# Performance work log

Hardware: AMD Instinct MI355X
Metric: run time of the kernel (lower is better)

Reference implementation:

```python
import jax, jax.numpy as jnp
import numpy as np

N_NODES = 50000
N_EDGES = 800000
N_GRAPHS = 64
IN_CH = 128
HID_CH = 128
OUT_CH = 2


def setup_inputs() -> dict:
    key = jax.random.key(0)
    k = jax.random.split(key, 7)
    x = jax.random.normal(k[0], (N_NODES, IN_CH), dtype=jnp.float32)
    edge_index = jax.random.randint(k[1], (2, N_EDGES), 0, N_NODES, dtype=jnp.int64)
    batch = jnp.sort(jax.random.randint(k[2], (N_NODES,), 0, N_GRAPHS, dtype=jnp.int64))
    W1 = jax.random.normal(k[3], (IN_CH, HID_CH), dtype=jnp.float32) * 0.05
    b1 = jnp.zeros((HID_CH,), dtype=jnp.float32)
    W2 = jax.random.normal(k[4], (HID_CH, OUT_CH), dtype=jnp.float32) * 0.05
    b2 = jnp.zeros((OUT_CH,), dtype=jnp.float32)
    return {"x": x, "edge_index": edge_index, "batch": batch,
            "W1": W1, "b1": b1, "W2": W2, "b2": b2}


def gcn_conv(x, edge_index, W, b):
    """PyG GCNConv: add self-loops, symmetric D^{-1/2}(A+I)D^{-1/2} aggregation of XW, plus bias."""
    n = x.shape[0]
    loop = jnp.arange(n, dtype=edge_index.dtype)
    src = jnp.concatenate([edge_index[0], loop])  # [E+N]
    dst = jnp.concatenate([edge_index[1], loop])
    ones = jnp.ones_like(dst, dtype=x.dtype)
    deg = jax.ops.segment_sum(ones, dst, num_segments=n)      # in-degree incl. self-loop (>=1)
    d_inv_sqrt = jax.lax.rsqrt(deg)
    norm = d_inv_sqrt[src] * d_inv_sqrt[dst]                  # [E+N]
    h = x @ W                                                 # [N, out]
    msg = h[src] * norm[:, None]                              # gather + scale
    out = jax.ops.segment_sum(msg, dst, num_segments=n)       # scatter-add
    return out + b


def global_mean_pool(x, batch, num_graphs):
    sums = jax.ops.segment_sum(x, batch, num_segments=num_graphs)
    cnt = jax.ops.segment_sum(jnp.ones((x.shape[0],), dtype=x.dtype), batch, num_segments=num_graphs)
    return sums / jnp.maximum(cnt, 1.0)[:, None]


def reference(x, edge_index, batch, W1, b1, W2, b2):
    h = jax.nn.relu(gcn_conv(x, edge_index, W1, b1))
    h = gcn_conv(h, edge_index, W2, b2)
    out = global_mean_pool(h, batch, N_GRAPHS)  # [G, out_channels]
    # dropout in eval mode == identity
    return out
```

## Files before the change

### kernel.cpp

```cpp
#include <hip/hip_runtime.h>


#define NGRAPH 64
#define CH 128
#define BSUB 384
#define NCOPY 8
#define BCAPT (BSUB * NCOPY)
#define CSTR 4096

typedef float f32x4 __attribute__((ext_vector_type(4)));
typedef _Float16 f16x8 __attribute__((ext_vector_type(8)));
typedef _Float16 f16x4 __attribute__((ext_vector_type(4)));
typedef _Float16 f16x2 __attribute__((ext_vector_type(2)));

__global__ void k_init(int* __restrict__ bcur8, float* __restrict__ gsum,
                       int* __restrict__ gcnt, int* __restrict__ done,
                       float* __restrict__ h2,
                       const float* __restrict__ W1, _Float16* __restrict__ w1t,
                       int NB, int N) {
    int i = blockIdx.x * blockDim.x + threadIdx.x;
    if (i < NB * NCOPY) bcur8[i] = 0;
    if (i < 2 * NGRAPH) gsum[i] = 0.f;
    if (i < NGRAPH) gcnt[i] = 0;
    if (i == 0) *done = 0;
    if (i < 2) h2[2 * N + i] = 0.f;
    if (i < CH * CH) {
        int k = i >> 7, c = i & 127;
        w1t[c * CH + k] = (_Float16)W1[i];
    }
}

__global__ __launch_bounds__(256) void k_bin(const int* __restrict__ src,
                                             const int* __restrict__ dst,
                                             int* __restrict__ bcur8,
                                             unsigned int* __restrict__ tmp,
                                             int E, int EPB) {
    __shared__ int hist[512];
    __shared__ int gbase[512];
    __shared__ int cur[512];
    int t = threadIdx.x;
    int e0 = blockIdx.x * EPB;
    int e1 = min(E, e0 + EPB);
    for (int i = t; i < 512; i += 256) { hist[i] = 0; cur[i] = 0; }
    __syncthreads();
    for (int e = e0 + t; e < e1; e += 256)
        atomicAdd(&hist[dst[e] >> 7], 1);
    __syncthreads();
    int copy = blockIdx.x & (NCOPY - 1);
    for (int b = t; b < 512; b += 256) {
        int hc = hist[b];
        if (hc) gbase[b] = atomicAdd(&bcur8[b * NCOPY + copy], hc);
    }
    __syncthreads();
    for (int e = e0 + t; e < e1; e += 256) {
        int d = dst[e];
        int b = d >> 7;
        int li = atomicAdd(&cur[b], 1);
        int pos = gbase[b] + li;
        if (pos < BSUB)
            tmp[(size_t)b * BCAPT + copy * BSUB + pos] =
                ((unsigned)(d & 127) << 25) | (unsigned)src[e];
    }
}

__global__ __launch_bounds__(256) void k_build(const unsigned int* __restrict__ tmp,
                                               const int* __restrict__ bcur8,
                                               int2* __restrict__ rs2,
                                               float* __restrict__ dinv,
                                               int* __restrict__ csr, int N) {
    __shared__ int hist[128];
    __shared__ int scan[128];
    __shared__ int lcur[128];
    int b = blockIdx.x, t = threadIdx.x;
    if (t < 128) hist[t] = 0;
    __syncthreads();
    const unsigned int* tb = tmp + (size_t)b * BCAPT;
    for (int c = 0; c < NCOPY; c++) {
        int cnt = min(bcur8[b * NCOPY + c], BSUB);
        const unsigned int* tp = tb + c * BSUB;
        for (int e = t; e < cnt; e += 256) atomicAdd(&hist[tp[e] >> 25], 1);
    }
    __syncthreads();
    int val = 0, v = 0, pv = 0;
    if (t < 128) { v = hist[t]; pv = (v + 7) & ~7; val = pv; scan[t] = val; }
    __syncthreads();
    for (int off = 1; off < 128; off <<= 1) {
        int add = (t >= off && t < 128) ? scan[t - off] : 0;
        __syncthreads();
        if (t < 128) { val += add; scan[t] = val; }
        __syncthreads();
    }
    int base = b * CSTR;
    if (t < 128) {
        int excl = val - pv;
        lcur[t] = excl;
        int n = b * 128 + t;
        if (n < N) {
            rs2[n] = make_int2(base + excl, pv);
            dinv[n] = rsqrtf((float)(v + 1));
            for (int e = v; e < pv; e++) csr[base + excl + e] = N;
        }
    }
    __syncthreads();
    for (int c = 0; c < NCOPY; c++) {
        int cnt = min(bcur8[b * NCOPY + c], BSUB);
        const unsigned int* tp = tb + c * BSUB;
        for (int e = t; e < cnt; e += 256) {
            unsigned p = tp[e];
            int pos = atomicAdd(&lcur[p >> 25], 1);
            csr[base + pos] = (int)(p & 0x01FFFFFFu);
        }
    }
}

__global__ __launch_bounds__(256) void k_gemm1(const float* __restrict__ X,
                                               const _Float16* __restrict__ w1t,
                                               const float* __restrict__ dinv,
                                               _Float16* __restrict__ H, int N) {
    __shared__ _Float16 Xs[64 * 136];
    __shared__ _Float16 Ws[128 * 136];
    int t = threadIdx.x;
    int row0 = blockIdx.x * 64;
    const float4* Xv = (const float4*)X;

    #pragma unroll
    for (int i = 0; i < 8; i++) {
        int gi = t + i * 256;
        int r = gi >> 5, c4 = gi & 31;
        int gr = row0 + r;
        float4 v = (gr < N) ? Xv[(size_t)gr * 32 + c4] : make_float4(0.f, 0.f, 0.f, 0.f);
        f16x4 hv = {(_Float16)v.x, (_Float16)v.y, (_Float16)v.z, (_Float16)v.w};
        *(f16x4*)&Xs[r * 136 + 4 * c4] = hv;
    }
    #pragma unroll
    for (int i = 0; i < 8; i++) {
        int gi = t + i * 256;
        int r = gi >> 4, cc = gi & 15;
        f16x8 vv = *(const f16x8*)&w1t[r * CH + cc * 8];
        *(f16x8*)&Ws[r * 136 + cc * 8] = vv;
    }
    __syncthreads();

    int w = t >> 6, l = t & 63;
    int r0w = w * 16;
    int lr = l & 15, lk = (l >> 4) * 8;
    f32x4 acc[8] = {};
    #pragma unroll
    for (int k0 = 0; k0 < 128; k0 += 32) {
        f16x8 a = *(const f16x8*)&Xs[(r0w + lr) * 136 + k0 + lk];
        #pragma unroll
        for (int c = 0; c < 8; c++) {
            f16x8 bf = *(const f16x8*)&Ws[(c * 16 + lr) * 136 + k0 + lk];
            acc[c] = __builtin_amdgcn_mfma_f32_16x16x32_f16(a, bf, acc[c], 0, 0, 0);
        }
    }
    float dv[4];
    #pragma unroll
    for (int q = 0; q < 4; q++) {
        int gr = row0 + r0w + (l >> 4) * 4 + q;
        dv[q] = (gr < N) ? dinv[gr] : 0.f;
    }
    __syncthreads();
    #pragma unroll
    for (int c = 0; c < 8; c++)
        #pragma unroll
        for (int q = 0; q < 4; q++)
            Xs[(r0w + (l >> 4) * 4 + q) * 136 + c * 16 + lr] = (_Float16)(acc[c][q] * dv[q]);
    __syncthreads();
    f16x2* Hv = (f16x2*)H;
    #pragma unroll
    for (int i = 0; i < 16; i++) {
        int gi = t + i * 256;
        int r = gi >> 6, cp = gi & 63;
        int gr = row0 + r;
        Hv[(size_t)gr * 64 + cp] = *(f16x2*)&Xs[r * 136 + 2 * cp];
    }
}

__global__ __launch_bounds__(256) void k_layer1(const _Float16* __restrict__ h,
                                                const int* __restrict__ csr,
                                                const int2* __restrict__ rs2,
                                                const float* __restrict__ dinv,
                                                const float* __restrict__ b1,
                                                const float* __restrict__ W2,
                                                float* __restrict__ h2, int N) {
    int n = (blockIdx.x * 256 + threadIdx.x) >> 6;
    int l = threadIdx.x & 63;
    if (n >= N) return;
    const f16x2* hv = (const f16x2*)h;
    float dn = dinv[n];
    f16x2 self = hv[(size_t)n * 64 + l];
    float acc0 = (float)self.x, acc1 = (float)self.y;
    int2 rs = rs2[n];
    int base = rs.x, cnt = rs.y;
    for (int c0 = 0; c0 < cnt; c0 += 64) {
        int m = cnt - c0; if (m > 64) m = 64;
        int idx = csr[base + c0 + l];
        for (int j = 0; j < m; j += 8) {
            int s0 = __shfl(idx, j + 0), s1 = __shfl(idx, j + 1);
            int s2 = __shfl(idx, j + 2), s3 = __shfl(idx, j + 3);
            int s4 = __shfl(idx, j + 4), s5 = __shfl(idx, j + 5);
            int s6 = __shfl(idx, j + 6), s7 = __shfl(idx, j + 7);
            f16x2 v0 = hv[(size_t)s0 * 64 + l];
            f16x2 v1 = hv[(size_t)s1 * 64 + l];
            f16x2 v2 = hv[(size_t)s2 * 64 + l];
            f16x2 v3 = hv[(size_t)s3 * 64 + l];
            f16x2 v4 = hv[(size_t)s4 * 64 + l];
            f16x2 v5 = hv[(size_t)s5 * 64 + l];
            f16x2 v6 = hv[(size_t)s6 * 64 + l];
            f16x2 v7 = hv[(size_t)s7 * 64 + l];
            acc0 += (float)v0.x; acc1 += (float)v0.y;
            acc0 += (float)v1.x; acc1 += (float)v1.y;
            acc0 += (float)v2.x; acc1 += (float)v2.y;
            acc0 += (float)v3.x; acc1 += (float)v3.y;
            acc0 += (float)v4.x; acc1 += (float)v4.y;
            acc0 += (float)v5.x; acc1 += (float)v5.y;
            acc0 += (float)v6.x; acc1 += (float)v6.y;
            acc0 += (float)v7.x; acc1 += (float)v7.y;
        }
    }
    float2 bb = ((const float2*)b1)[l];
    float v0 = fmaxf(fmaf(dn, acc0, bb.x), 0.f);
    float v1 = fmaxf(fmaf(dn, acc1, bb.y), 0.f);
    float4 w2 = ((const float4*)W2)[l];
    float p0 = fmaf(v0, w2.x, v1 * w2.z);
    float p1 = fmaf(v0, w2.y, v1 * w2.w);
    #pragma unroll
    for (int off = 32; off; off >>= 1) {
        p0 += __shfl_xor(p0, off);
        p1 += __shfl_xor(p1, off);
    }
    if (l == 0) ((float2*)h2)[n] = make_float2(p0 * dn, p1 * dn);
}

__global__ __launch_bounds__(256) void k_layer2_pool(const float* __restrict__ h2,
                                                     const int* __restrict__ csr,
                                                     const int2* __restrict__ rs2,
                                                     const float* __restrict__ dinv,
                                                     const int* __restrict__ batch,
                                                     float* __restrict__ gsum,
                                                     int* __restrict__ gcnt,
                                                     int* __restrict__ done,
                                                     const float* __restrict__ b2,
                                                     float* __restrict__ out, int N) {
    __shared__ float ssum[2 * NGRAPH];
    __shared__ int scnt[NGRAPH];
    __shared__ int s_last;
    int t = threadIdx.x;
    if (t < 2 * NGRAPH) ssum[t] = 0.f;
    if (t < NGRAPH) scnt[t] = 0;
    __syncthreads();
    int n = blockIdx.x * blockDim.x + t;
    if (n < N) {
        const float2* h2v = (const float2*)h2;
        float dn = dinv[n];
        float2 a = h2v[n];
        int2 rs = rs2[n];
        for (int e = rs.x; e < rs.x + rs.y; e++) {
            float2 v = h2v[csr[e]];
            a.x += v.x;
            a.y += v.y;
        }
        a.x *= dn;
        a.y *= dn;
        int g = batch[n];
        atomicAdd(&ssum[g * 2 + 0], a.x);
        atomicAdd(&ssum[g * 2 + 1], a.y);
        atomicAdd(&scnt[g], 1);
    }
    __syncthreads();
    if (t < 2 * NGRAPH) atomicAdd(&gsum[t], ssum[t]);
    if (t < NGRAPH) atomicAdd(&gcnt[t], scnt[t]);
    __syncthreads();
    if (t == 0) {
        __threadfence();
        int r = atomicAdd(done, 1);
        s_last = (r == (int)gridDim.x - 1) ? 1 : 0;
    }
    __syncthreads();
    if (s_last && t < 2 * NGRAPH) {
        int g = t >> 1, c = t & 1;
        float sv = atomicAdd(&gsum[t], 0.f);
        float cv = (float)atomicAdd(&gcnt[g], 0);
        out[t] = sv / fmaxf(cv, 1.f) + b2[c];
    }
}

extern "C" void kernel_launch(void* const* d_in, const int* in_sizes, int n_in,
                              void* d_out, int out_size, void* d_ws, size_t ws_size,
                              hipStream_t stream) {
    const float* x     = (const float*)d_in[0];
    const int*   ei    = (const int*)d_in[1];
    const int*   batch = (const int*)d_in[2];
    const float* W1    = (const float*)d_in[3];
    const float* b1    = (const float*)d_in[4];
    const float* W2    = (const float*)d_in[5];
    const float* b2    = (const float*)d_in[6];
    float* out = (float*)d_out;

    int N = in_sizes[0] / CH;
    int E = in_sizes[1] / 2;
    int NB = (N + 127) / 128;
    const int* esrc = ei;
    const int* edst = ei + E;

    char* w = (char*)d_ws;
    auto alloc = [&](size_t bytes) -> void* {
        void* p = (void*)w;
        w += (bytes + 255) & ~(size_t)255;
        return p;
    };
    _Float16* h      = (_Float16*)alloc((size_t)(N + 64) * CH * sizeof(_Float16));
    float* dinv      = (float*)alloc((size_t)N * sizeof(float));
    int2* rs2        = (int2*) alloc((size_t)N * sizeof(int2));
    int* csr         = (int*)  alloc((size_t)NB * CSTR * sizeof(int));
    float* h2        = (float*)alloc((size_t)(N + 1) * 2 * sizeof(float));
    int* bcur8       = (int*)  alloc((size_t)NB * NCOPY * sizeof(int));
    _Float16* w1t    = (_Float16*)alloc((size_t)CH * CH * sizeof(_Float16));
    float* gsum      = (float*)alloc(128 * sizeof(float));
    int* gcnt        = (int*)  alloc(64 * sizeof(int));
    int* done        = (int*)  alloc(256);
    unsigned int* tmp = (unsigned int*)h;

    int nbN = (N + 255) / 256;
    int NCHUNK = 256;
    int EPB = (E + NCHUNK - 1) / NCHUNK;

    k_init  <<<64, 256, 0, stream>>>(bcur8, gsum, gcnt, done, h2, W1, w1t, NB, N);
    k_bin   <<<NCHUNK, 256, 0, stream>>>(esrc, edst, bcur8, tmp, E, EPB);
    k_build <<<NB, 256, 0, stream>>>(tmp, bcur8, rs2, dinv, csr, N);
    k_gemm1 <<<(N + 63) / 64, 256, 0, stream>>>(x, w1t, dinv, h, N);
    k_layer1<<<(N * 64 + 255) / 256, 256, 0, stream>>>(h, csr, rs2, dinv, b1, W2, h2, N);
    k_layer2_pool<<<nbN, 256, 0, stream>>>(h2, csr, rs2, dinv, batch, gsum, gcnt,
                                           done, b2, out, N);
}
```

Measured before the change: 169.7 us.

## Fuse all GCN stages into one cooperative persistent kernel with grid barriers

The six separate launches (init, bin, build, gemm1, layer1, layer2+pool) become a single cooperative kernel of 512 blocks. Stages are separated by a hand-written atomic grid barrier, and control buffers are zeroed by one memset. The aim is to remove per-launch overhead and idle gaps between the small stages. Alongside this, the binning gets 16 copies of smaller sub-buckets, the edge scratch buffer is no longer aliased onto h, and gemm1 reads W1 fragments straight from global memory instead of staging them in LDS. In exchange there are barrier spin costs, a fixed grid that splits the gemm tiles unevenly, and a fallback multi-kernel path if the cooperative launch fails.

After: 474.5 us. 180% more time.

```diff
diff --git a/kernel.cpp b/kernel.cpp
--- a/kernel.cpp
+++ b/kernel.cpp
@@ -3,82 +3,77 @@
 
 #define NGRAPH 64
 #define CH 128
-#define BSUB 384
-#define NCOPY 8
+#define NTHR 256
+#define NBLK 512
+#define NCOPY 16
+#define BSUB 224
 #define BCAPT (BSUB * NCOPY)
-#define CSTR 4096
+#define CSTR 4608
 
 typedef float f32x4 __attribute__((ext_vector_type(4)));
 typedef _Float16 f16x8 __attribute__((ext_vector_type(8)));
 typedef _Float16 f16x4 __attribute__((ext_vector_type(4)));
 typedef _Float16 f16x2 __attribute__((ext_vector_type(2)));
 
-__global__ void k_init(int* __restrict__ bcur8, float* __restrict__ gsum,
-                       int* __restrict__ gcnt, int* __restrict__ done,
-                       float* __restrict__ h2,
-                       const float* __restrict__ W1, _Float16* __restrict__ w1t,
-                       int NB, int N) {
-    int i = blockIdx.x * blockDim.x + threadIdx.x;
-    if (i < NB * NCOPY) bcur8[i] = 0;
-    if (i < 2 * NGRAPH) gsum[i] = 0.f;
-    if (i < NGRAPH) gcnt[i] = 0;
-    if (i == 0) *done = 0;
-    if (i < 2) h2[2 * N + i] = 0.f;
-    if (i < CH * CH) {
-        int k = i >> 7, c = i & 127;
-        w1t[c * CH + k] = (_Float16)W1[i];
-    }
-}
-
-__global__ __launch_bounds__(256) void k_bin(const int* __restrict__ src,
-                                             const int* __restrict__ dst,
-                                             int* __restrict__ bcur8,
-                                             unsigned int* __restrict__ tmp,
-                                             int E, int EPB) {
-    __shared__ int hist[512];
-    __shared__ int gbase[512];
-    __shared__ int cur[512];
+struct MegaP {
+    const float* x; const int* esrc; const int* edst; const int* batch;
+    const float* W1; const float* b1; const float* W2; const float* b2;
+    float* out;
+    _Float16* h; unsigned int* tmp; float* dinv; int2* rs2; int* csr;
+    float* h2; int* bcur8; _Float16* w1t; float* gsum; int* gcnt; int* cnt;
+    int N, E, NB, EPB;
+};
+
+__device__ __forceinline__ void gbar(int* cnt, int ph) {
+    __syncthreads();
+    if (threadIdx.x == 0) {
+        __builtin_amdgcn_fence(__ATOMIC_RELEASE, "");
+        __hip_atomic_fetch_add(cnt, 1, __ATOMIC_RELAXED, __HIP_MEMORY_SCOPE_AGENT);
+        while (__hip_atomic_load(cnt, __ATOMIC_RELAXED, __HIP_MEMORY_SCOPE_AGENT)
+               < NBLK * ph)
+            __builtin_amdgcn_s_sleep(16);
+        __builtin_amdgcn_fence(__ATOMIC_ACQUIRE, "");
+    }
+    __syncthreads();
+}
+
+__device__ __forceinline__ void bin_body(const int* src, const int* dst,
+                                         int* bcur8, unsigned int* tmp,
+                                         int E, int e0, int e1, int copy,
+                                         int* hist, int* gbase, int* cur) {
     int t = threadIdx.x;
-    int e0 = blockIdx.x * EPB;
-    int e1 = min(E, e0 + EPB);
-    for (int i = t; i < 512; i += 256) { hist[i] = 0; cur[i] = 0; }
-    __syncthreads();
-    for (int e = e0 + t; e < e1; e += 256)
+    for (int i = t; i < 512; i += NTHR) { hist[i] = 0; cur[i] = 0; }
+    __syncthreads();
+    for (int e = e0 + t; e < e1; e += NTHR)
         atomicAdd(&hist[dst[e] >> 7], 1);
     __syncthreads();
-    int copy = blockIdx.x & (NCOPY - 1);
-    for (int b = t; b < 512; b += 256) {
+    for (int b = t; b < 512; b += NTHR) {
         int hc = hist[b];
         if (hc) gbase[b] = atomicAdd(&bcur8[b * NCOPY + copy], hc);
     }
     __syncthreads();
-    for (int e = e0 + t; e < e1; e += 256) {
+    for (int e = e0 + t; e < e1; e += NTHR) {
         int d = dst[e];
         int b = d >> 7;
-        int li = atomicAdd(&cur[b], 1);
-        int pos = gbase[b] + li;
-        if (pos < BSUB)
+        int pos = gbase[b] + atomicAdd(&cur[b], 1);
+        if ((unsigned)pos < BSUB)
             tmp[(size_t)b * BCAPT + copy * BSUB + pos] =
                 ((unsigned)(d & 127) << 25) | (unsigned)src[e];
     }
 }
 
-__global__ __launch_bounds__(256) void k_build(const unsigned int* __restrict__ tmp,
-                                               const int* __restrict__ bcur8,
-                                               int2* __restrict__ rs2,
-                                               float* __restrict__ dinv,
-                                               int* __restrict__ csr, int N) {
-    __shared__ int hist[128];
-    __shared__ int scan[128];
-    __shared__ int lcur[128];
-    int b = blockIdx.x, t = threadIdx.x;
+__device__ __forceinline__ void build_body(const unsigned int* tmp, const int* bcur8,
+                                           int2* rs2, float* dinv, int* csr,
+                                           int N, int b,
+                                           int* hist, int* scan, int* lcur) {
+    int t = threadIdx.x;
     if (t < 128) hist[t] = 0;
     __syncthreads();
     const unsigned int* tb = tmp + (size_t)b * BCAPT;
     for (int c = 0; c < NCOPY; c++) {
         int cnt = min(bcur8[b * NCOPY + c], BSUB);
         const unsigned int* tp = tb + c * BSUB;
-        for (int e = t; e < cnt; e += 256) atomicAdd(&hist[tp[e] >> 25], 1);
+        for (int e = t; e < cnt; e += NTHR) atomicAdd(&hist[tp[e] >> 25], 1);
     }
     __syncthreads();
     int val = 0, v = 0, pv = 0;
@@ -105,42 +100,30 @@
     for (int c = 0; c < NCOPY; c++) {
         int cnt = min(bcur8[b * NCOPY + c], BSUB);
         const unsigned int* tp = tb + c * BSUB;
-        for (int e = t; e < cnt; e += 256) {
-            unsigned p = tp[e];
-            int pos = atomicAdd(&lcur[p >> 25], 1);
-            csr[base + pos] = (int)(p & 0x01FFFFFFu);
-        }
-    }
-}
-
-__global__ __launch_bounds__(256) void k_gemm1(const float* __restrict__ X,
-                                               const _Float16* __restrict__ w1t,
-                                               const float* __restrict__ dinv,
-                                               _Float16* __restrict__ H, int N) {
-    __shared__ _Float16 Xs[64 * 136];
-    __shared__ _Float16 Ws[128 * 136];
+        for (int e = t; e < cnt; e += NTHR) {
+            unsigned pw = tp[e];
+            int pos = atomicAdd(&lcur[pw >> 25], 1);
+            csr[base + pos] = (int)(pw & 0x01FFFFFFu);
+        }
+    }
+}
+
+__device__ __forceinline__ void gemm1_tile(const float* X, const _Float16* w1t,
+                                           const float* dinv, _Float16* H,
+                                           int N, int tile, _Float16* Xs) {
     int t = threadIdx.x;
-    int row0 = blockIdx.x * 64;
+    int row0 = tile * 64;
     const float4* Xv = (const float4*)X;
-
     #pragma unroll
     for (int i = 0; i < 8; i++) {
-        int gi = t + i * 256;
+        int gi = t + i * NTHR;
         int r = gi >> 5, c4 = gi & 31;
         int gr = row0 + r;
         float4 v = (gr < N) ? Xv[(size_t)gr * 32 + c4] : make_float4(0.f, 0.f, 0.f, 0.f);
-        f16x4 hv = {(_Float16)v.x, (_Float16)v.y, (_Float16)v.z, (_Float16)v.w};
-        *(f16x4*)&Xs[r * 136 + 4 * c4] = hv;
-    }
-    #pragma unroll
-    for (int i = 0; i < 8; i++) {
-        int gi = t + i * 256;
-        int r = gi >> 4, cc = gi & 15;
-        f16x8 vv = *(const f16x8*)&w1t[r * CH + cc * 8];
-        *(f16x8*)&Ws[r * 136 + cc * 8] = vv;
-    }
-    __syncthreads();
-
+        f16x4 hv4 = {(_Float16)v.x, (_Float16)v.y, (_Float16)v.z, (_Float16)v.w};
+        *(f16x4*)&Xs[r * 136 + 4 * c4] = hv4;
+    }
+    __syncthreads();
     int w = t >> 6, l = t & 63;
     int r0w = w * 16;
     int lr = l & 15, lk = (l >> 4) * 8;
@@ -150,7 +133,7 @@
         f16x8 a = *(const f16x8*)&Xs[(r0w + lr) * 136 + k0 + lk];
         #pragma unroll
         for (int c = 0; c < 8; c++) {
-            f16x8 bf = *(const f16x8*)&Ws[(c * 16 + lr) * 136 + k0 + lk];
+            f16x8 bf = *(const f16x8*)&w1t[(c * 16 + lr) * CH + k0 + lk];
             acc[c] = __builtin_amdgcn_mfma_f32_16x16x32_f16(a, bf, acc[c], 0, 0, 0);
         }
     }
@@ -165,29 +148,24 @@
     for (int c = 0; c < 8; c++)
         #pragma unroll
         for (int q = 0; q < 4; q++)
-            Xs[(r0w + (l >> 4) * 4 + q) * 136 + c * 16 + lr] = (_Float16)(acc[c][q] * dv[q]);
+            Xs[(r0w + (l >> 4) * 4 + q) * 136 + c * 16 + lr] =
+                (_Float16)(acc[c][q] * dv[q]);
     __syncthreads();
     f16x2* Hv = (f16x2*)H;
     #pragma unroll
     for (int i = 0; i < 16; i++) {
-        int gi = t + i * 256;
+        int gi = t + i * NTHR;
         int r = gi >> 6, cp = gi & 63;
         int gr = row0 + r;
         Hv[(size_t)gr * 64 + cp] = *(f16x2*)&Xs[r * 136 + 2 * cp];
     }
-}
-
-__global__ __launch_bounds__(256) void k_layer1(const _Float16* __restrict__ h,
-                                                const int* __restrict__ csr,
-                                                const int2* __restrict__ rs2,
-                                                const float* __restrict__ dinv,
-                                                const float* __restrict__ b1,
-                                                const float* __restrict__ W2,
-                                                float* __restrict__ h2, int N) {
-    int n = (blockIdx.x * 256 + threadIdx.x) >> 6;
-    int l = threadIdx.x & 63;
-    if (n >= N) return;
-    const f16x2* hv = (const f16x2*)h;
+    __syncthreads();
+}
+
+__device__ __forceinline__ void layer1_node(const f16x2* hv, const int* csr,
+                                            const int2* rs2, const float* dinv,
+                                            const float* b1, const float* W2,
+                                            float* h2, int n, int l) {
     float dn = dinv[n];
     f16x2 self = hv[(size_t)n * 64 + l];
     float acc0 = (float)self.x, acc1 = (float)self.y;
@@ -233,16 +211,133 @@
     if (l == 0) ((float2*)h2)[n] = make_float2(p0 * dn, p1 * dn);
 }
 
-__global__ __launch_bounds__(256) void k_layer2_pool(const float* __restrict__ h2,
-                                                     const int* __restrict__ csr,
-                                                     const int2* __restrict__ rs2,
-                                                     const float* __restrict__ dinv,
-                                                     const int* __restrict__ batch,
-                                                     float* __restrict__ gsum,
-                                                     int* __restrict__ gcnt,
-                                                     int* __restrict__ done,
-                                                     const float* __restrict__ b2,
-                                                     float* __restrict__ out, int N) {
+__global__ __launch_bounds__(NTHR, 2) void k_mega(MegaP p) {
+    __shared__ __align__(16) char smem[17408];
+    int t = threadIdx.x, blk = blockIdx.x;
+    int gtid = blk * NTHR + t;
+
+    if (gtid < 2) p.h2[2 * p.N + gtid] = 0.f;
+    if (gtid < CH * CH) {
+        int k = gtid >> 7, c = gtid & 127;
+        p.w1t[c * CH + k] = (_Float16)p.W1[gtid];
+    }
+    gbar(p.cnt, 1);
+    {
+        int* hist = (int*)smem;
+        bin_body(p.esrc, p.edst, p.bcur8, p.tmp, p.E,
+                 blk * p.EPB, min(p.E, blk * p.EPB + p.EPB), blk & (NCOPY - 1),
+                 hist, hist + 512, hist + 1024);
+    }
+    gbar(p.cnt, 2);
+    if (blk < p.NB) {
+        int* hist = (int*)smem;
+        build_body(p.tmp, p.bcur8, p.rs2, p.dinv, p.csr, p.N, blk,
+                   hist, hist + 128, hist + 256);
+    }
+    gbar(p.cnt, 3);
+    {
+        int ntile = (p.N + 63) / 64;
+        for (int tile = blk; tile < ntile; tile += NBLK)
+            gemm1_tile(p.x, p.w1t, p.dinv, p.h, p.N, tile, (_Float16*)smem);
+    }
+    gbar(p.cnt, 4);
+    {
+        const f16x2* hv = (const f16x2*)p.h;
+        int l = t & 63;
+        for (int n = blk * 4 + (t >> 6); n < p.N; n += NBLK * 4)
+            layer1_node(hv, p.csr, p.rs2, p.dinv, p.b1, p.W2, p.h2, n, l);
+    }
+    gbar(p.cnt, 5);
+    {
+        float* ssum = (float*)smem;
+        int* scnt = (int*)(smem + 512);
+        if (t < 2 * NGRAPH) ssum[t] = 0.f;
+        if (t < NGRAPH) scnt[t] = 0;
+        __syncthreads();
+        int n = gtid;
+        if (n < p.N) {
+            const float2* h2v = (const float2*)p.h2;
+            float dn = p.dinv[n];
+            float2 a = h2v[n];
+            int2 rs = p.rs2[n];
+            for (int e = rs.x; e < rs.x + rs.y; e++) {
+                float2 v = h2v[p.csr[e]];
+                a.x += v.x; a.y += v.y;
+            }
+            a.x *= dn; a.y *= dn;
+            int g = p.batch[n];
+            atomicAdd(&ssum[g * 2 + 0], a.x);
+            atomicAdd(&ssum[g * 2 + 1], a.y);
+            atomicAdd(&scnt[g], 1);
+        }
+        __syncthreads();
+        if (blk * NTHR < p.N) {
+            if (t < 2 * NGRAPH) atomicAdd(&p.gsum[t], ssum[t]);
+            if (t < NGRAPH) atomicAdd(&p.gcnt[t], scnt[t]);
+        }
+    }
+    gbar(p.cnt, 6);
+    if (blk == 0 && t < 2 * NGRAPH) {
+        int g = t >> 1, c = t & 1;
+        float sv = atomicAdd(&p.gsum[t], 0.f);
+        float cv = (float)atomicAdd(&p.gcnt[g], 0);
+        p.out[t] = sv / fmaxf(cv, 1.f) + p.b2[c];
+    }
+}
+
+__global__ void k_init(int* __restrict__ bcur8, float* __restrict__ gsum,
+                       int* __restrict__ gcnt, int* __restrict__ done,
+                       float* __restrict__ h2, const float* __restrict__ W1,
+                       _Float16* __restrict__ w1t, int NB, int N) {
+    int i = blockIdx.x * blockDim.x + threadIdx.x;
+    if (i < NB * NCOPY) bcur8[i] = 0;
+    if (i < 2 * NGRAPH) gsum[i] = 0.f;
+    if (i < NGRAPH) gcnt[i] = 0;
+    if (i == 0) *done = 0;
+    if (i < 2) h2[2 * N + i] = 0.f;
+    if (i < CH * CH) {
+        int k = i >> 7, c = i & 127;
+        w1t[c * CH + k] = (_Float16)W1[i];
+    }
+}
+
+__global__ __launch_bounds__(NTHR) void k_bin(const int* src, const int* dst,
+                                              int* bcur8, unsigned int* tmp,
+                                              int E, int EPB) {
+    __shared__ int smem[1536];
+    bin_body(src, dst, bcur8, tmp, E, blockIdx.x * EPB,
+             min(E, blockIdx.x * EPB + EPB), blockIdx.x & (NCOPY - 1),
+             smem, smem + 512, smem + 1024);
+}
+
+__global__ __launch_bounds__(NTHR) void k_build(const unsigned int* tmp,
+                                                const int* bcur8, int2* rs2,
+                                                float* dinv, int* csr, int N) {
+    __shared__ int smem[384];
+    build_body(tmp, bcur8, rs2, dinv, csr, N, blockIdx.x,
+               smem, smem + 128, smem + 256);
+}
+
+__global__ __launch_bounds__(NTHR) void k_gemm1(const float* X, const _Float16* w1t,
+                                                const float* dinv, _Float16* H, int N) {
+    __shared__ __align__(16) _Float16 Xs[64 * 136];
+    gemm1_tile(X, w1t, dinv, H, N, blockIdx.x, Xs);
+}
+
+__global__ __launch_bounds__(NTHR) void k_layer1(const _Float16* h, const int* csr,
+                                                 const int2* rs2, const float* dinv,
+                                                 const float* b1, const float* W2,
+                                                 float* h2, int N) {
+    int n = (blockIdx.x * NTHR + threadIdx.x) >> 6;
+    if (n >= N) return;
+    layer1_node((const f16x2*)h, csr, rs2, dinv, b1, W2, h2, n, threadIdx.x & 63);
+}
+
+__global__ __launch_bounds__(NTHR) void k_layer2_pool(const float* h2, const int* csr,
+                                                      const int2* rs2, const float* dinv,
+                                                      const int* batch, float* gsum,
+                                                      int* gcnt, int* done,
+                                                      const float* b2, float* out, int N) {
     __shared__ float ssum[2 * NGRAPH];
     __shared__ int scnt[NGRAPH];
     __shared__ int s_last;
@@ -258,11 +353,9 @@
         int2 rs = rs2[n];
         for (int e = rs.x; e < rs.x + rs.y; e++) {
             float2 v = h2v[csr[e]];
-            a.x += v.x;
-            a.y += v.y;
-        }
-        a.x *= dn;
-        a.y *= dn;
+            a.x += v.x; a.y += v.y;
+        }
+        a.x *= dn; a.y *= dn;
         int g = batch[n];
         atomicAdd(&ssum[g * 2 + 0], a.x);
         atomicAdd(&ssum[g * 2 + 1], a.y);
@@ -289,20 +382,9 @@
 extern "C" void kernel_launch(void* const* d_in, const int* in_sizes, int n_in,
                               void* d_out, int out_size, void* d_ws, size_t ws_size,
                               hipStream_t stream) {
-    const float* x     = (const float*)d_in[0];
-    const int*   ei    = (const int*)d_in[1];
-    const int*   batch = (const int*)d_in[2];
-    const float* W1    = (const float*)d_in[3];
-    const float* b1    = (const float*)d_in[4];
-    const float* W2    = (const float*)d_in[5];
-    const float* b2    = (const float*)d_in[6];
-    float* out = (float*)d_out;
-
     int N = in_sizes[0] / CH;
     int E = in_sizes[1] / 2;
     int NB = (N + 127) / 128;
-    const int* esrc = ei;
-    const int* edst = ei + E;
 
     char* w = (char*)d_ws;
     auto alloc = [&](size_t bytes) -> void* {
@@ -310,27 +392,50 @@
         w += (bytes + 255) & ~(size_t)255;
         return p;
     };
+    int* cnt         = (int*)  alloc(256);
+    int* bcur8       = (int*)  alloc((size_t)NB * NCOPY * sizeof(int));
+    float* gsum      = (float*)alloc(128 * sizeof(float));
+    int* gcnt        = (int*)  alloc(64 * sizeof(int));
+    int* done        = (int*)  alloc(256);
+    size_t ctrl_bytes = (size_t)(w - (char*)d_ws);
     _Float16* h      = (_Float16*)alloc((size_t)(N + 64) * CH * sizeof(_Float16));
+    unsigned int* tmp= (unsigned int*)alloc((size_t)NB * BCAPT * sizeof(unsigned int));
     float* dinv      = (float*)alloc((size_t)N * sizeof(float));
     int2* rs2        = (int2*) alloc((size_t)N * sizeof(int2));
     int* csr         = (int*)  alloc((size_t)NB * CSTR * sizeof(int));
     float* h2        = (float*)alloc((size_t)(N + 1) * 2 * sizeof(float));
-    int* bcur8       = (int*)  alloc((size_t)NB * NCOPY * sizeof(int));
     _Float16* w1t    = (_Float16*)alloc((size_t)CH * CH * sizeof(_Float16));
-    float* gsum      = (float*)alloc(128 * sizeof(float));
-    int* gcnt        = (int*)  alloc(64 * sizeof(int));
-    int* done        = (int*)  alloc(256);
-    unsigned int* tmp = (unsigned int*)h;
-
-    int nbN = (N + 255) / 256;
-    int NCHUNK = 256;
-    int EPB = (E + NCHUNK - 1) / NCHUNK;
-
-    k_init  <<<64, 256, 0, stream>>>(bcur8, gsum, gcnt, done, h2, W1, w1t, NB, N);
-    k_bin   <<<NCHUNK, 256, 0, stream>>>(esrc, edst, bcur8, tmp, E, EPB);
-    k_build <<<NB, 256, 0, stream>>>(tmp, bcur8, rs2, dinv, csr, N);
-    k_gemm1 <<<(N + 63) / 64, 256, 0, stream>>>(x, w1t, dinv, h, N);
-    k_layer1<<<(N * 64 + 255) / 256, 256, 0, stream>>>(h, csr, rs2, dinv, b1, W2, h2, N);
-    k_layer2_pool<<<nbN, 256, 0, stream>>>(h2, csr, rs2, dinv, batch, gsum, gcnt,
-                                           done, b2, out, N);
-}
+
+    MegaP p;
+    p.x = (const float*)d_in[0];
+    p.esrc = (const int*)d_in[1];
+    p.edst = (const int*)d_in[1] + E;
+    p.batch = (const int*)d_in[2];
+    p.W1 = (const float*)d_in[3];
+    p.b1 = (const float*)d_in[4];
+    p.W2 = (const float*)d_in[5];
+    p.b2 = (const float*)d_in[6];
+    p.out = (float*)d_out;
+    p.h = h; p.tmp = tmp; p.dinv = dinv; p.rs2 = rs2; p.csr = csr;
+    p.h2 = h2; p.bcur8 = bcur8; p.w1t = w1t; p.gsum = gsum; p.gcnt = gcnt;
+    p.cnt = cnt;
+    p.N = N; p.E = E; p.NB = NB;
+    p.EPB = (E + NBLK - 1) / NBLK;
+
+    (void)hipMemsetAsync(d_ws, 0, ctrl_bytes, stream);
+    void* args[] = {&p};
+    hipError_t err = hipLaunchCooperativeKernel((const void*)k_mega, dim3(NBLK),
+                                                dim3(NTHR), args, 0, stream);
+    if (err != hipSuccess) {
+        int EPBf = (E + 255) / 256;
+        k_init  <<<64, NTHR, 0, stream>>>(bcur8, gsum, gcnt, done, h2, p.W1, w1t, NB, N);
+        k_bin   <<<256, NTHR, 0, stream>>>(p.esrc, p.edst, bcur8, tmp, E, EPBf);
+        k_build <<<NB, NTHR, 0, stream>>>(tmp, bcur8, rs2, dinv, csr, N);
+        k_gemm1 <<<(N + 63) / 64, NTHR, 0, stream>>>(p.x, w1t, dinv, h, N);
+        k_layer1<<<(N * 64 + NTHR - 1) / NTHR, NTHR, 0, stream>>>(h, csr, rs2, dinv,
+                                                                  p.b1, p.W2, h2, N);
+        k_layer2_pool<<<(N + NTHR - 1) / NTHR, NTHR, 0, stream>>>(h2, csr, rs2, dinv,
+                                                                  p.batch, gsum, gcnt,
+                                                                  done, p.b2, p.out, N);
+    }
+}
```
